# Kernel tuning notes

Hardware: AMD Instinct MI355X
Metric: run time of the kernel (lower is better)

The kernel has to match this reference:

```python
import jax, jax.numpy as jnp
import numpy as np

B, N_PER, E_PER = 100, 1000, 12000  # graphs, nodes/graph, edges/graph
N, E = B * N_PER, B * E_PER
K = int(np.ceil(0.8 * N_PER))  # TopKPooling ratio=0.8 -> 800 kept nodes/graph


def setup_inputs() -> dict:
    key = jax.random.key(0)
    ks = jax.random.split(key, 16)
    g = jnp.repeat(jnp.arange(B, dtype=jnp.int64), E_PER)
    src = g * N_PER + jax.random.randint(ks[0], (E,), 0, N_PER)
    dst = g * N_PER + jax.random.randint(ks[1], (E,), 0, N_PER)
    edge_index = jnp.stack([src, dst]).astype(jnp.int64)
    edge_attr = jax.random.uniform(ks[2], (E,), dtype=jnp.float32) + 0.1  # positive edge weights
    x = jax.random.normal(ks[3], (N, 3), dtype=jnp.float32)
    batch = jnp.repeat(jnp.arange(B, dtype=jnp.int64), N_PER)
    s = 0.1
    return {
        'x': x, 'edge_index': edge_index, 'edge_attr': edge_attr, 'batch': batch,
        'conv1_w': jax.random.normal(ks[4], (3, 64), dtype=jnp.float32) * s,
        'conv1_b': jnp.zeros((64,), dtype=jnp.float32),
        'conv2_w': jax.random.normal(ks[5], (64, 64), dtype=jnp.float32) * s,
        'conv2_b': jnp.zeros((64,), dtype=jnp.float32),
        'pool_w': jax.random.normal(ks[6], (64,), dtype=jnp.float32) * s,
        'lin1_w': jax.random.normal(ks[7], (64, 64), dtype=jnp.float32) * s,
        'lin1_b': jnp.zeros((64,), dtype=jnp.float32),
        'lin2_w': jax.random.normal(ks[8], (64, 32), dtype=jnp.float32) * s,
        'lin2_b': jnp.zeros((32,), dtype=jnp.float32),
        'lin3_w': jax.random.normal(ks[9], (32, 1), dtype=jnp.float32) * s,
        'lin3_b': jnp.zeros((1,), dtype=jnp.float32),
    }


def gcn_conv(x, row, col, ew, W, b):
    # PyG GCNConv with edge_weight and implicit self-loops (weight 1):
    # deg[i] = sum_{e: col=i} ew[e] + 1;  norm_e = d^{-1/2}[row]*ew*d^{-1/2}[col]
    h = x @ W  # [N, out]
    deg = jax.ops.segment_sum(ew, col, num_segments=N) + 1.0
    dinv = jax.lax.rsqrt(deg)
    msg = (dinv[row] * ew * dinv[col])[:, None] * h[row]  # [E, out]
    out = jax.ops.segment_sum(msg, col, num_segments=N)
    out = out + (dinv * dinv)[:, None] * h  # self-loop term
    return out + b


def reference(x, edge_index, edge_attr, batch, conv1_w, conv1_b, conv2_w, conv2_b,
              pool_w, lin1_w, lin1_b, lin2_w, lin2_b, lin3_w, lin3_b):
    row, col = edge_index[0], edge_index[1]
    h = jax.nn.relu(gcn_conv(x, row, col, edge_attr, conv1_w, conv1_b))
    x1 = h.reshape(B, N_PER, 64).mean(axis=1)  # global_mean_pool (equal-size graphs)
    h = jax.nn.relu(gcn_conv(h, row, col, edge_attr, conv2_w, conv2_b))
    # TopKPooling: score = tanh(x.w / ||w||), keep top-K per graph, gate by score
    score = jnp.tanh(h @ pool_w / jnp.linalg.norm(pool_w))  # [N]
    score_bn = score.reshape(B, N_PER)
    vals, idx = jax.lax.top_k(score_bn, K)  # [B, K]
    h_bn = h.reshape(B, N_PER, 64)
    h_sel = jnp.take_along_axis(h_bn, idx[..., None], axis=1) * vals[..., None]
    x2 = h_sel.mean(axis=1)  # global_mean_pool on pooled graph
    z = x1 + x2
    z = jax.nn.relu(z @ lin1_w + lin1_b)
    z = jax.nn.relu(z @ lin2_w + lin2_b)  # dropout is identity in eval mode
    out = jax.nn.sigmoid(z @ lin3_w + lin3_b)[:, 0]
    return out
```

## Files before the change

kernel.cpp:

```cpp
#include <hip/hip_runtime.h>

#define B_G   100
#define N_PER 1000
#define E_PER 12000
#define NTOT  (B_G * N_PER)
#define ETOT  (B_G * E_PER)
#define KSEL  800
#define EPT   12

typedef __attribute__((ext_vector_type(8))) short short8;
typedef __attribute__((ext_vector_type(4))) float float4_;

__device__ __forceinline__ unsigned short f2bf(float f) {
    unsigned u = __float_as_uint(f);
    u += 0x7fffu + ((u >> 16) & 1u);
    return (unsigned short)(u >> 16);
}
__device__ __forceinline__ float upk(unsigned q) {
    return __uint_as_float(q & 0xFFFF0000u);
}
__device__ __forceinline__ float dec_raw(unsigned byte7f) {
    return __uint_as_float(byte7f << 20);
}
__device__ __forceinline__ unsigned enc_fp8(float z) {
    unsigned u = __float_as_uint(z * 0x1p-120f);
    u += 0x7FFFFu + ((u >> 20) & 1u);
    return u >> 20;
}

__global__ __launch_bounds__(1024) void k_all(
    const int* __restrict__ ei, const float* __restrict__ ew,
    const float* __restrict__ x,
    const float* __restrict__ w1, const float* __restrict__ b1,
    const float* __restrict__ w2, const float* __restrict__ b2,
    const float* __restrict__ pw,
    const float* __restrict__ l1w, const float* __restrict__ l1b,
    const float* __restrict__ l2w, const float* __restrict__ l2b,
    const float* __restrict__ l3w, const float* __restrict__ l3b,
    unsigned char* __restrict__ h2g, float* __restrict__ out) {
    __shared__ __align__(16) unsigned char smem[145024];
    unsigned char* zs = smem;
    float* xl = (float*)smem;
    unsigned* csr = (unsigned*)(smem + 64000);
    int*   ends = (int*)(smem + 112000);
    float* dl   = (float*)(smem + 116096);
    int*   posc = (int*)(smem + 116096);
    int*   wpart = (int*)(smem + 120192);
    float* x1b   = (float*)(smem + 120192);
    unsigned char* uA = smem + 120448;
    float* aggv = (float*)uA;
    unsigned short* w2s = (unsigned short*)(smem + 136832);

    int b = blockIdx.x, tid = threadIdx.x;
    int wid = tid >> 6, lane = tid & 63;
    int gbase = b * N_PER, ebase = b * E_PER;

    int esrc[EPT], edst[EPT]; float eww[EPT];
    int ne = (tid < (E_PER - (EPT - 1) * 1024)) ? EPT : EPT - 1;
#pragma unroll
    for (int i = 0; i < EPT; i++) {
        if (i < ne) {
            int e = tid + i * 1024;
            esrc[i] = ei[ebase + e] - gbase;
            edst[i] = ei[ETOT + ebase + e] - gbase;
            eww[i]  = ew[ebase + e];
        }
    }
    ends[tid] = 0;
    for (int i = tid; i < N_PER * 3; i += 1024) xl[i] = x[(size_t)gbase * 3 + i];
    {
        int n = tid >> 4;
        for (int k = (tid & 15) * 4, ke = k + 4; k < ke; k++)
            w2s[n * 64 + k] = f2bf(w2[k * 64 + n]);
    }
    __syncthreads();
#pragma unroll
    for (int i = 0; i < EPT; i++)
        if (i < ne) atomicAdd(&ends[edst[i]], 1);
    __syncthreads();
    int v = ends[tid];
    int sc = v;
#pragma unroll
    for (int m = 1; m < 64; m <<= 1) {
        int t = __shfl_up(sc, m);
        if (lane >= m) sc += t;
    }
    if (lane == 63) wpart[wid] = sc;
    __syncthreads();
    if (tid < 16) {
        int s2 = wpart[tid];
#pragma unroll
        for (int m = 1; m < 16; m <<= 1) {
            int t = __shfl_up(s2, m);
            if (tid >= m) s2 += t;
        }
        wpart[tid] = s2;
    }
    __syncthreads();
    int incl = sc + (wid > 0 ? wpart[wid - 1] : 0);
    ends[tid] = incl;
    posc[tid] = incl - v;
    __syncthreads();
#pragma unroll
    for (int i = 0; i < EPT; i++)
        if (i < ne) {
            int p = atomicAdd(&posc[edst[i]], 1);
            csr[p] = ((unsigned)f2bf(eww[i]) << 16) | (unsigned)esrc[i];
        }
    __syncthreads();
    float dmy = 0.f;
    int s0i = 0, e0i = 0;
    if (tid < N_PER) {
        s0i = tid ? ends[tid - 1] : 0;
        e0i = ends[tid];
        float s0 = 0.f, s1 = 0.f;
        int k = s0i;
        for (; k + 2 <= e0i; k += 2) { s0 += upk(csr[k]); s1 += upk(csr[k + 1]); }
        if (k < e0i) s0 += upk(csr[k]);
        dmy = rsqrtf(s0 + s1 + 1.0f);
        dl[tid] = dmy;
        xl[tid * 3 + 0] *= dmy;
        xl[tid * 3 + 1] *= dmy;
        xl[tid * 3 + 2] *= dmy;
    }
    __syncthreads();
    if (tid < N_PER) {
        float a0 = xl[tid * 3 + 0], a1 = xl[tid * 3 + 1], a2 = xl[tid * 3 + 2];
        for (int k = s0i; k < e0i; k++) {
            unsigned q = csr[k];
            int i0 = (int)(q & 0xFFFFu) * 3;
            float wv = upk(q);
            a0 += wv * xl[i0]; a1 += wv * xl[i0 + 1]; a2 += wv * xl[i0 + 2];
        }
        aggv[tid * 3 + 0] = dmy * a0;
        aggv[tid * 3 + 1] = dmy * a1;
        aggv[tid * 3 + 2] = dmy * a2;
    }
    __syncthreads();
    {
        float w0 = w1[lane], w1v = w1[64 + lane], w2v = w1[128 + lane], bf = b1[lane];
        float* sred = (float*)(uA + 12288);
        float px = 0.f;
        int chunk = (lane & 31) >> 3;
        int word  = ((lane >= 32) ? 2 : 0) + ((lane & 7) >> 2);
        for (int node = wid; node < N_PER; node += 16) {
            float a0 = aggv[node * 3], a1 = aggv[node * 3 + 1], a2 = aggv[node * 3 + 2];
            float hv = fmaxf(a0 * w0 + a1 * w1v + a2 * w2v + bf, 0.f);
            px += hv;
            unsigned byte = enc_fp8(dl[node] * hv);
            unsigned t1 = __shfl_xor(byte, 1);
            unsigned v16 = (lane & 1) ? (t1 | (byte << 8)) : (byte | (t1 << 8));
            unsigned t2 = __shfl_xor(v16, 2);
            unsigned v32 = (lane & 2) ? (t2 | (v16 << 16)) : (v16 | (t2 << 16));
            if ((lane & 3) == 0) {
                int cs = chunk ^ ((node >> 1) & 3);
                *(unsigned*)(zs + node * 64 + cs * 16 + word * 4) = v32;
            }
        }
        sred[wid * 64 + lane] = px;
        __syncthreads();
        if (tid < 64) {
            float t = 0.f;
            for (int r = 0; r < 16; r++) t += sred[r * 64 + tid];
            x1b[tid] = t * (1.0f / N_PER);
        }
    }
    int kgrp = lane >> 4, nloc = lane & 15;
    unsigned long long* keys = (unsigned long long*)uA;
    if (tid >= N_PER) keys[tid] = 0ull;
    float b2c[4], pwc[4];
#pragma unroll
    for (int c = 0; c < 4; ++c) {
        b2c[c] = b2[c * 16 + nloc];
        pwc[c] = pw[c * 16 + nloc];
    }
    float invn;
    {
        float p = pw[lane], pn = p * p;
#pragma unroll
        for (int m = 32; m; m >>= 1) pn += __shfl_xor(pn, m);
        invn = rsqrtf(pn);
    }
#pragma unroll 1
    for (int ti = 0; ti < 4; ti++) {
        int t = wid + ti * 16;
        if (t >= 63) continue;
        int li = t * 16 + nloc;
        bool valid = li < N_PER;
        float acc[16];
        int s = 0, cn = 0;
        if (valid) {
            uint4 rv = *(const uint4*)(zs + li * 64 + ((kgrp ^ ((li >> 1) & 3)) << 4));
#pragma unroll
            for (int j = 0; j < 4; j++) {
                acc[j]      = dec_raw((rv.x >> (8 * j)) & 0x7Fu);
                acc[4 + j]  = dec_raw((rv.y >> (8 * j)) & 0x7Fu);
                acc[8 + j]  = dec_raw((rv.z >> (8 * j)) & 0x7Fu);
                acc[12 + j] = dec_raw((rv.w >> (8 * j)) & 0x7Fu);
            }
            s = li ? ends[li - 1] : 0;
            cn = ends[li] - s;
        } else {
#pragma unroll
            for (int j = 0; j < 16; j++) acc[j] = 0.f;
        }
        int mx = cn;
#pragma unroll
        for (int m = 1; m < 16; m <<= 1) mx = max(mx, __shfl_xor(mx, m));
        for (int k = 0; k < mx; k++) {
            if (k < cn) {
                unsigned q = csr[s + k];
                int src = (int)(q & 0xFFFFu);
                float wv = upk(q);
                uint4 rv = *(const uint4*)(zs + src * 64 + ((kgrp ^ ((src >> 1) & 3)) << 4));
#pragma unroll
                for (int j = 0; j < 4; j++) {
                    acc[j]      += wv * dec_raw((rv.x >> (8 * j)) & 0x7Fu);
                    acc[4 + j]  += wv * dec_raw((rv.y >> (8 * j)) & 0x7Fu);
                    acc[8 + j]  += wv * dec_raw((rv.z >> (8 * j)) & 0x7Fu);
                    acc[12 + j] += wv * dec_raw((rv.w >> (8 * j)) & 0x7Fu);
                }
            }
        }
        float scale = (valid ? dl[li] : 0.f) * 0x1p120f;
        short8 Af0, Af1;
#pragma unroll
        for (int j = 0; j < 8; j++) {
            Af0[j] = (short)f2bf(scale * acc[j]);
            Af1[j] = (short)f2bf(scale * acc[8 + j]);
        }
        float4_ accv[4];
#pragma unroll
        for (int c = 0; c < 4; ++c) {
            const short8* bp = (const short8*)(w2s + (c * 16 + nloc) * 64 + kgrp * 8);
            accv[c] = __builtin_amdgcn_mfma_f32_16x16x32_bf16(Af0, bp[0], (float4_){0.f,0.f,0.f,0.f}, 0, 0, 0);
            accv[c] = __builtin_amdgcn_mfma_f32_16x16x32_bf16(Af1, bp[4], accv[c], 0, 0, 0);
        }
#pragma unroll
        for (int r2 = 0; r2 < 4; ++r2) {
            int li2 = t * 16 + kgrp * 4 + r2;
            bool valid2 = li2 < N_PER;
            float sp = 0.f;
            unsigned pack = 0;
#pragma unroll
            for (int c = 0; c < 4; ++c) {
                float hv = fmaxf(accv[c][r2] + b2c[c], 0.f);
                sp += hv * pwc[c];
                pack |= enc_fp8(hv) << (8 * c);
            }
            if (valid2)
                *(unsigned*)(h2g + (size_t)(gbase + li2) * 64 + nloc * 4) = pack;
#pragma unroll
            for (int m = 1; m < 16; m <<= 1) sp += __shfl_xor(sp, m);
            if (valid2 && nloc == 0) {
                float scv = tanhf(sp * invn);
                unsigned bits = __float_as_uint(scv);
                unsigned u = (bits & 0x80000000u) ? ~bits : (bits | 0x80000000u);
                keys[li2] = ((unsigned long long)u << 32) | (unsigned)(1023 - li2);
            }
        }
    }
    __syncthreads();
    {
        unsigned long long key = keys[tid];
        for (int k = 2; k <= 1024; k <<= 1) {
            for (int j = k >> 1; j > 0; j >>= 1) {
                bool desc = (tid & k) == 0;
                unsigned long long p;
                if (j >= 64) {
                    keys[tid] = key;
                    __syncthreads();
                    p = keys[tid ^ j];
                    __syncthreads();
                } else {
                    p = __shfl_xor(key, j);
                }
                bool low = (tid & j) == 0;
                bool sw = low ? (desc ? (key < p) : (key > p))
                              : (desc ? (p < key) : (p > key));
                if (sw) key = p;
            }
        }
        keys[tid] = key;
    }
    __syncthreads();
    float* red   = (float*)(uA + 8192);
    float* a1buf = (float*)(uA + 12288);
    float* a2buf = (float*)(uA + 12544);
    float* zbuf  = (float*)(uA + 12672);
    {
        int f = tid & 63, w16 = tid >> 6;
        int boff = ((f & 15) << 2) + (f >> 4);
        float acc2 = 0.f;
        for (int r = w16; r < KSEL; r += 16) {
            unsigned long long key = keys[r];
            int idx = 1023 - (int)(key & 0xFFFFFFFFu);
            unsigned u = (unsigned)(key >> 32);
            unsigned bits = (u & 0x80000000u) ? (u & 0x7FFFFFFFu) : ~u;
            float valS = __uint_as_float(bits) * 0x1p120f;
            acc2 += valS * dec_raw((unsigned)h2g[(size_t)(gbase + idx) * 64 + boff] & 0x7Fu);
        }
        red[tid] = acc2;
    }
    __syncthreads();
    if (tid < 64) {
        float s2 = 0.f;
        for (int ww = 0; ww < 16; ww++) s2 += red[ww * 64 + tid];
        zbuf[tid] = x1b[tid] + s2 * (1.0f / KSEL);
    }
    __syncthreads();
    if (tid < 64) {
        float a = l1b[tid];
        for (int k = 0; k < 64; k++) a += zbuf[k] * l1w[k * 64 + tid];
        a1buf[tid] = fmaxf(a, 0.f);
    }
    __syncthreads();
    if (tid < 32) {
        float a = l2b[tid];
        for (int k = 0; k < 64; k++) a += a1buf[k] * l2w[k * 32 + tid];
        a2buf[tid] = fmaxf(a, 0.f);
    }
    __syncthreads();
    if (tid == 0) {
        float t = l3b[0];
        for (int k = 0; k < 32; k++) t += a2buf[k] * l3w[k];
        out[b] = 1.0f / (1.0f + expf(-t));
    }
}

extern "C" void kernel_launch(void* const* d_in, const int* in_sizes, int n_in,
                              void* d_out, int out_size, void* d_ws, size_t ws_size,
                              hipStream_t stream) {
    const float* x   = (const float*)d_in[0];
    const int*   ei  = (const int*)d_in[1];
    const float* ew  = (const float*)d_in[2];
    const float* c1w = (const float*)d_in[4];
    const float* c1b = (const float*)d_in[5];
    const float* c2w = (const float*)d_in[6];
    const float* c2b = (const float*)d_in[7];
    const float* pw  = (const float*)d_in[8];
    const float* l1w = (const float*)d_in[9];
    const float* l1b = (const float*)d_in[10];
    const float* l2w = (const float*)d_in[11];
    const float* l2b = (const float*)d_in[12];
    const float* l3w = (const float*)d_in[13];
    const float* l3b = (const float*)d_in[14];
    float* out = (float*)d_out;
    unsigned char* h2g = (unsigned char*)d_ws;
    (void)ws_size; (void)in_sizes; (void)n_in; (void)out_size;

    k_all<<<B_G, 1024, 0, stream>>>(ei, ew, x, c1w, c1b, c2w, c2b, pw,
                                    l1w, l1b, l2w, l2b, l3w, l3b, h2g, out);
}
```

Baseline: 192.6 us.

## Split fused per-graph kernel into four stages, conv2 over two blocks per graph

Breaks the single fused per-graph kernel into four launches: CSR build, conv1, conv2 and top-k with the MLP. The conv2 stage runs two blocks per graph, each handling half the nodes, so the 100-block grid becomes 200 blocks and uses more of the GPU's compute units. The cost is extra global-memory round trips for the CSR, the fp8 activations, degrees and scores, plus three more kernel launches. Each conv2 block also reloads the full 64 KB activation tile.

Measured after the change: 189.7 us. Within noise of the previous version (-1.5%).

```diff
diff --git a/kernel.cpp b/kernel.cpp
--- a/kernel.cpp
+++ b/kernel.cpp
@@ -7,6 +7,8 @@
 #define ETOT  (B_G * E_PER)
 #define KSEL  800
 #define EPT   12
+#define NH    500
+#define HCAP  8192
 
 typedef __attribute__((ext_vector_type(8))) short short8;
 typedef __attribute__((ext_vector_type(4))) float float4_;
@@ -28,29 +30,14 @@
     return u >> 20;
 }
 
-__global__ __launch_bounds__(1024) void k_all(
+__global__ __launch_bounds__(1024) void k1_build(
     const int* __restrict__ ei, const float* __restrict__ ew,
-    const float* __restrict__ x,
-    const float* __restrict__ w1, const float* __restrict__ b1,
-    const float* __restrict__ w2, const float* __restrict__ b2,
-    const float* __restrict__ pw,
-    const float* __restrict__ l1w, const float* __restrict__ l1b,
-    const float* __restrict__ l2w, const float* __restrict__ l2b,
-    const float* __restrict__ l3w, const float* __restrict__ l3b,
-    unsigned char* __restrict__ h2g, float* __restrict__ out) {
-    __shared__ __align__(16) unsigned char smem[145024];
-    unsigned char* zs = smem;
-    float* xl = (float*)smem;
-    unsigned* csr = (unsigned*)(smem + 64000);
-    int*   ends = (int*)(smem + 112000);
-    float* dl   = (float*)(smem + 116096);
-    int*   posc = (int*)(smem + 116096);
-    int*   wpart = (int*)(smem + 120192);
-    float* x1b   = (float*)(smem + 120192);
-    unsigned char* uA = smem + 120448;
-    float* aggv = (float*)uA;
-    unsigned short* w2s = (unsigned short*)(smem + 136832);
-
+    unsigned* __restrict__ csr_g, int* __restrict__ ends_g,
+    float* __restrict__ dl_g) {
+    __shared__ unsigned csr[E_PER];
+    __shared__ int ends[1024];
+    __shared__ int posc[1024];
+    __shared__ int wpart[16];
     int b = blockIdx.x, tid = threadIdx.x;
     int wid = tid >> 6, lane = tid & 63;
     int gbase = b * N_PER, ebase = b * E_PER;
@@ -67,19 +54,12 @@
         }
     }
     ends[tid] = 0;
-    for (int i = tid; i < N_PER * 3; i += 1024) xl[i] = x[(size_t)gbase * 3 + i];
-    {
-        int n = tid >> 4;
-        for (int k = (tid & 15) * 4, ke = k + 4; k < ke; k++)
-            w2s[n * 64 + k] = f2bf(w2[k * 64 + n]);
-    }
     __syncthreads();
 #pragma unroll
     for (int i = 0; i < EPT; i++)
         if (i < ne) atomicAdd(&ends[edst[i]], 1);
     __syncthreads();
-    int v = ends[tid];
-    int sc = v;
+    int v = ends[tid], sc = v;
 #pragma unroll
     for (int m = 1; m < 64; m <<= 1) {
         int t = __shfl_up(sc, m);
@@ -108,41 +88,68 @@
             csr[p] = ((unsigned)f2bf(eww[i]) << 16) | (unsigned)esrc[i];
         }
     __syncthreads();
-    float dmy = 0.f;
-    int s0i = 0, e0i = 0;
     if (tid < N_PER) {
-        s0i = tid ? ends[tid - 1] : 0;
-        e0i = ends[tid];
+        int s = tid ? ends[tid - 1] : 0, e = ends[tid];
         float s0 = 0.f, s1 = 0.f;
-        int k = s0i;
-        for (; k + 2 <= e0i; k += 2) { s0 += upk(csr[k]); s1 += upk(csr[k + 1]); }
-        if (k < e0i) s0 += upk(csr[k]);
-        dmy = rsqrtf(s0 + s1 + 1.0f);
-        dl[tid] = dmy;
-        xl[tid * 3 + 0] *= dmy;
-        xl[tid * 3 + 1] *= dmy;
-        xl[tid * 3 + 2] *= dmy;
-    }
-    __syncthreads();
+        int k = s;
+        for (; k + 2 <= e; k += 2) { s0 += upk(csr[k]); s1 += upk(csr[k + 1]); }
+        if (k < e) s0 += upk(csr[k]);
+        dl_g[gbase + tid] = rsqrtf(s0 + s1 + 1.0f);
+        ends_g[gbase + tid] = e;
+    }
+    for (int i = tid; i < E_PER; i += 1024)
+        csr_g[(size_t)ebase + i] = csr[i];
+}
+
+__global__ __launch_bounds__(1024) void k2_conv1(
+    const float* __restrict__ x,
+    const float* __restrict__ w1, const float* __restrict__ b1,
+    const unsigned* __restrict__ csr_g, const int* __restrict__ ends_g,
+    const float* __restrict__ dl_g,
+    unsigned char* __restrict__ zg, float* __restrict__ x1g) {
+    __shared__ float xl[3000];
+    __shared__ unsigned csr[E_PER];
+    __shared__ int ends[1024];
+    __shared__ float dl[1024];
+    __shared__ float aggv[3000];
+    __shared__ float sred[1024];
+    int b = blockIdx.x, tid = threadIdx.x;
+    int wid = tid >> 6, lane = tid & 63;
+    int gbase = b * N_PER, ebase = b * E_PER;
+
+    for (int i = tid; i < N_PER * 3; i += 1024) xl[i] = x[(size_t)gbase * 3 + i];
+    for (int i = tid; i < E_PER; i += 1024) csr[i] = csr_g[(size_t)ebase + i];
     if (tid < N_PER) {
+        ends[tid] = ends_g[gbase + tid];
+        dl[tid] = dl_g[gbase + tid];
+    }
+    __syncthreads();
+    if (tid < N_PER) {
+        float d = dl[tid];
+        xl[tid * 3 + 0] *= d; xl[tid * 3 + 1] *= d; xl[tid * 3 + 2] *= d;
+    }
+    __syncthreads();
+    if (tid < N_PER) {
+        int s = tid ? ends[tid - 1] : 0, e = ends[tid];
         float a0 = xl[tid * 3 + 0], a1 = xl[tid * 3 + 1], a2 = xl[tid * 3 + 2];
-        for (int k = s0i; k < e0i; k++) {
+        for (int k = s; k < e; k++) {
             unsigned q = csr[k];
             int i0 = (int)(q & 0xFFFFu) * 3;
             float wv = upk(q);
             a0 += wv * xl[i0]; a1 += wv * xl[i0 + 1]; a2 += wv * xl[i0 + 2];
         }
-        aggv[tid * 3 + 0] = dmy * a0;
-        aggv[tid * 3 + 1] = dmy * a1;
-        aggv[tid * 3 + 2] = dmy * a2;
+        float d = dl[tid];
+        aggv[tid * 3 + 0] = d * a0;
+        aggv[tid * 3 + 1] = d * a1;
+        aggv[tid * 3 + 2] = d * a2;
     }
     __syncthreads();
     {
         float w0 = w1[lane], w1v = w1[64 + lane], w2v = w1[128 + lane], bf = b1[lane];
-        float* sred = (float*)(uA + 12288);
         float px = 0.f;
         int chunk = (lane & 31) >> 3;
         int word  = ((lane >= 32) ? 2 : 0) + ((lane & 7) >> 2);
+        unsigned char* zrow = zg + (size_t)b * 64000;
         for (int node = wid; node < N_PER; node += 16) {
             float a0 = aggv[node * 3], a1 = aggv[node * 3 + 1], a2 = aggv[node * 3 + 2];
             float hv = fmaxf(a0 * w0 + a1 * w1v + a2 * w2v + bf, 0.f);
@@ -154,7 +161,7 @@
             unsigned v32 = (lane & 2) ? (t2 | (v16 << 16)) : (v16 | (t2 << 16));
             if ((lane & 3) == 0) {
                 int cs = chunk ^ ((node >> 1) & 3);
-                *(unsigned*)(zs + node * 64 + cs * 16 + word * 4) = v32;
+                *(unsigned*)(zrow + node * 64 + cs * 16 + word * 4) = v32;
             }
         }
         sred[wid * 64 + lane] = px;
@@ -162,12 +169,44 @@
         if (tid < 64) {
             float t = 0.f;
             for (int r = 0; r < 16; r++) t += sred[r * 64 + tid];
-            x1b[tid] = t * (1.0f / N_PER);
-        }
-    }
+            x1g[b * 64 + tid] = t * (1.0f / N_PER);
+        }
+    }
+}
+
+__global__ __launch_bounds__(1024) void k3_conv2(
+    const unsigned char* __restrict__ zg, const unsigned* __restrict__ csr_g,
+    const int* __restrict__ ends_g, const float* __restrict__ dl_g,
+    const float* __restrict__ w2, const float* __restrict__ b2,
+    const float* __restrict__ pw,
+    unsigned char* __restrict__ h2g, float* __restrict__ score_g) {
+    __shared__ __align__(16) unsigned char zs[64000];
+    __shared__ unsigned csr[HCAP];
+    __shared__ int ends[NH + 12];
+    __shared__ float dl[NH + 12];
+    __shared__ unsigned short w2s[64 * 64];
+    int blk = blockIdx.x;
+    int g = blk >> 1, h = blk & 1;
+    int tid = threadIdx.x, wid = tid >> 6, lane = tid & 63;
     int kgrp = lane >> 4, nloc = lane & 15;
-    unsigned long long* keys = (unsigned long long*)uA;
-    if (tid >= N_PER) keys[tid] = 0ull;
+    int gbase = g * N_PER, nbase = h * NH;
+
+    for (int i = tid; i < 64000 / 4; i += 1024)
+        ((unsigned*)zs)[i] = ((const unsigned*)(zg + (size_t)g * 64000))[i];
+    int base = h ? ends_g[gbase + NH - 1] : 0;
+    int etot = ends_g[gbase + nbase + NH - 1];
+    int nE = etot - base;
+    if (tid < NH) {
+        ends[tid] = ends_g[gbase + nbase + tid] - base;
+        dl[tid] = dl_g[gbase + nbase + tid];
+    }
+    for (int i = tid; i < nE; i += 1024)
+        csr[i] = csr_g[(size_t)g * E_PER + base + i];
+    {
+        int n = tid >> 4;
+        for (int k = (tid & 15) * 4, ke = k + 4; k < ke; k++)
+            w2s[n * 64 + k] = f2bf(w2[k * 64 + n]);
+    }
     float b2c[4], pwc[4];
 #pragma unroll
     for (int c = 0; c < 4; ++c) {
@@ -181,16 +220,17 @@
         for (int m = 32; m; m >>= 1) pn += __shfl_xor(pn, m);
         invn = rsqrtf(pn);
     }
+    __syncthreads();
 #pragma unroll 1
-    for (int ti = 0; ti < 4; ti++) {
+    for (int ti = 0; ti < 2; ti++) {
         int t = wid + ti * 16;
-        if (t >= 63) continue;
         int li = t * 16 + nloc;
-        bool valid = li < N_PER;
+        bool valid = li < NH;
         float acc[16];
         int s = 0, cn = 0;
         if (valid) {
-            uint4 rv = *(const uint4*)(zs + li * 64 + ((kgrp ^ ((li >> 1) & 3)) << 4));
+            int gn = nbase + li;
+            uint4 rv = *(const uint4*)(zs + gn * 64 + ((kgrp ^ ((gn >> 1) & 3)) << 4));
 #pragma unroll
             for (int j = 0; j < 4; j++) {
                 acc[j]      = dec_raw((rv.x >> (8 * j)) & 0x7Fu);
@@ -239,7 +279,7 @@
 #pragma unroll
         for (int r2 = 0; r2 < 4; ++r2) {
             int li2 = t * 16 + kgrp * 4 + r2;
-            bool valid2 = li2 < N_PER;
+            bool valid2 = li2 < NH;
             float sp = 0.f;
             unsigned pack = 0;
 #pragma unroll
@@ -249,16 +289,33 @@
                 pack |= enc_fp8(hv) << (8 * c);
             }
             if (valid2)
-                *(unsigned*)(h2g + (size_t)(gbase + li2) * 64 + nloc * 4) = pack;
+                *(unsigned*)(h2g + (size_t)(gbase + nbase + li2) * 64 + nloc * 4) = pack;
 #pragma unroll
             for (int m = 1; m < 16; m <<= 1) sp += __shfl_xor(sp, m);
-            if (valid2 && nloc == 0) {
-                float scv = tanhf(sp * invn);
-                unsigned bits = __float_as_uint(scv);
-                unsigned u = (bits & 0x80000000u) ? ~bits : (bits | 0x80000000u);
-                keys[li2] = ((unsigned long long)u << 32) | (unsigned)(1023 - li2);
-            }
-        }
+            if (valid2 && nloc == 0)
+                score_g[gbase + nbase + li2] = tanhf(sp * invn);
+        }
+    }
+}
+
+__global__ __launch_bounds__(1024) void k4_topk(
+    const float* __restrict__ score_g, const unsigned char* __restrict__ h2g,
+    const float* __restrict__ x1g,
+    const float* __restrict__ l1w, const float* __restrict__ l1b,
+    const float* __restrict__ l2w, const float* __restrict__ l2b,
+    const float* __restrict__ l3w, const float* __restrict__ l3b,
+    float* __restrict__ out) {
+    __shared__ unsigned long long keys[1024];
+    __shared__ float red[1024];
+    __shared__ float zbuf[64], a1buf[64], a2buf[32];
+    int b = blockIdx.x, tid = threadIdx.x;
+    if (tid < N_PER) {
+        float scv = score_g[b * N_PER + tid];
+        unsigned bits = __float_as_uint(scv);
+        unsigned u = (bits & 0x80000000u) ? ~bits : (bits | 0x80000000u);
+        keys[tid] = ((unsigned long long)u << 32) | (unsigned)(1023 - tid);
+    } else {
+        keys[tid] = 0ull;
     }
     __syncthreads();
     {
@@ -284,10 +341,6 @@
         keys[tid] = key;
     }
     __syncthreads();
-    float* red   = (float*)(uA + 8192);
-    float* a1buf = (float*)(uA + 12288);
-    float* a2buf = (float*)(uA + 12544);
-    float* zbuf  = (float*)(uA + 12672);
     {
         int f = tid & 63, w16 = tid >> 6;
         int boff = ((f & 15) << 2) + (f >> 4);
@@ -298,7 +351,7 @@
             unsigned u = (unsigned)(key >> 32);
             unsigned bits = (u & 0x80000000u) ? (u & 0x7FFFFFFFu) : ~u;
             float valS = __uint_as_float(bits) * 0x1p120f;
-            acc2 += valS * dec_raw((unsigned)h2g[(size_t)(gbase + idx) * 64 + boff] & 0x7Fu);
+            acc2 += valS * dec_raw((unsigned)h2g[(size_t)(b * N_PER + idx) * 64 + boff] & 0x7Fu);
         }
         red[tid] = acc2;
     }
@@ -306,7 +359,7 @@
     if (tid < 64) {
         float s2 = 0.f;
         for (int ww = 0; ww < 16; ww++) s2 += red[ww * 64 + tid];
-        zbuf[tid] = x1b[tid] + s2 * (1.0f / KSEL);
+        zbuf[tid] = x1g[b * 64 + tid] + s2 * (1.0f / KSEL);
     }
     __syncthreads();
     if (tid < 64) {
@@ -346,9 +399,21 @@
     const float* l3w = (const float*)d_in[13];
     const float* l3b = (const float*)d_in[14];
     float* out = (float*)d_out;
-    unsigned char* h2g = (unsigned char*)d_ws;
+
+    char* ws = (char*)d_ws;
+    size_t o = 0;
+    auto alloc = [&](size_t bytes) { size_t cur = o; o += (bytes + 511) & ~(size_t)511; return cur; };
+    unsigned*      csr_g   = (unsigned*)(ws + alloc((size_t)ETOT * 4));
+    unsigned char* zg      = (unsigned char*)(ws + alloc((size_t)NTOT * 64));
+    unsigned char* h2g     = (unsigned char*)(ws + alloc((size_t)NTOT * 64));
+    int*           ends_g  = (int*)(ws + alloc((size_t)NTOT * 4));
+    float*         dl_g    = (float*)(ws + alloc((size_t)NTOT * 4));
+    float*         score_g = (float*)(ws + alloc((size_t)NTOT * 4));
+    float*         x1g     = (float*)(ws + alloc((size_t)B_G * 64 * 4));
     (void)ws_size; (void)in_sizes; (void)n_in; (void)out_size;
 
-    k_all<<<B_G, 1024, 0, stream>>>(ei, ew, x, c1w, c1b, c2w, c2b, pw,
-                                    l1w, l1b, l2w, l2b, l3w, l3b, h2g, out);
-}
+    k1_build<<<B_G, 1024, 0, stream>>>(ei, ew, csr_g, ends_g, dl_g);
+    k2_conv1<<<B_G, 1024, 0, stream>>>(x, c1w, c1b, csr_g, ends_g, dl_g, zg, x1g);
+    k3_conv2<<<B_G * 2, 1024, 0, stream>>>(zg, csr_g, ends_g, dl_g, c2w, c2b, pw, h2g, score_g);
+    k4_topk <<<B_G, 1024, 0, stream>>>(score_g, h2g, x1g, l1w, l1b, l2w, l2b, l3w, l3b, out);
+}
```
